# Kernel optimization log

Hardware: AMD Instinct MI355X
Metric: run time of the kernel (lower is better)

The kernel has to match this reference:

```python
import jax, jax.numpy as jnp
import numpy as np
import math

NUM_HEADS = 12
EMBED_DIM = 768

def setup_inputs() -> dict:
    key = jax.random.key(0)
    ks = jax.random.split(key, 9)
    B, T, D = 2, 2048, EMBED_DIM
    s = 1.0 / math.sqrt(D)
    inp = {
        "x": jax.random.normal(ks[0], (B, T, D), dtype=jnp.float32),
        "Wq": jax.random.normal(ks[1], (D, D), dtype=jnp.float32) * s,
        "bq": jnp.zeros((D,), dtype=jnp.float32),
        "Wk": jax.random.normal(ks[2], (D, D), dtype=jnp.float32) * s,
        "bk": jnp.zeros((D,), dtype=jnp.float32),
        "Wv": jax.random.normal(ks[3], (D, D), dtype=jnp.float32) * s,
        "bv": jnp.zeros((D,), dtype=jnp.float32),
        "Wo": jax.random.normal(ks[4], (D, D), dtype=jnp.float32) * s,
        "bo": jnp.zeros((D,), dtype=jnp.float32),
    }
    return inp

def reference(x, Wq, bq, Wk, bk, Wv, bv, Wo, bo):
    B, T, D = x.shape
    H = NUM_HEADS
    Dh = D // H
    # QKV projections, split heads: [B, H, T, Dh]
    def proj(W, b):
        y = x @ W.T + b
        return y.reshape(B, T, H, Dh).transpose(0, 2, 1, 3)
    q = proj(Wq, bq)
    k = proj(Wk, bk)
    v = proj(Wv, bv)
    scores = jnp.einsum('bhtd,bhsd->bhts', q, k) / math.sqrt(Dh)  # [B,H,T,T]
    attn = jax.nn.softmax(scores, axis=-1)
    ctx = jnp.einsum('bhts,bhsd->bhtd', attn, v)  # [B,H,T,Dh]
    ctx = ctx.transpose(0, 2, 1, 3).reshape(B, T, D)
    out = ctx @ Wo.T + bo
    return out
```

## Files before the change

kernel.cpp:

```cpp
#include <hip/hip_runtime.h>
#include <math.h>

using f32x4   = __attribute__((ext_vector_type(4))) float;
using bf16x8  = __attribute__((ext_vector_type(8))) short;

constexpr int Bb = 2;
constexpr int T  = 2048;
constexpr int D  = 768;
constexpr int H  = 12;
constexpr int Dh = 64;
constexpr int M  = Bb * T;
constexpr int NQKV = 3 * D;
#define SCALE_Q 0.18033688011112042f

__device__ __forceinline__ unsigned short f2bf(float f) {
    unsigned u = __float_as_uint(f);
    u += 0x7fffu + ((u >> 16) & 1u);
    return (unsigned short)(u >> 16);
}

__device__ __forceinline__ ushort4 f2bf4(float4 f) {
    return make_ushort4(f2bf(f.x), f2bf(f.y), f2bf(f.z), f2bf(f.w));
}

__device__ __forceinline__ unsigned permpk(float hi_f, float lo_f) {
    return __builtin_amdgcn_perm(__float_as_uint(hi_f), __float_as_uint(lo_f),
                                 0x07060302u);
}

__device__ __forceinline__ void async_copy16(const void* g, void* lds_base) {
    __builtin_amdgcn_global_load_lds(
        (const __attribute__((address_space(1))) unsigned int*)g,
        (__attribute__((address_space(3))) unsigned int*)lds_base, 16, 0, 0);
}

__global__ __launch_bounds__(256) void prep_kernel(
    const float4* __restrict__ x,
    const float4* __restrict__ Wq, const float4* __restrict__ Wk,
    const float4* __restrict__ Wv, const float4* __restrict__ Wo,
    const float* __restrict__ bq, const float* __restrict__ bk, const float* __restrict__ bv,
    ushort4* __restrict__ Xb, ushort4* __restrict__ Wqkvb, ushort4* __restrict__ Wob,
    float* __restrict__ biasS)
{
    const int stride = gridDim.x * 256;
    const int i0 = blockIdx.x * 256 + threadIdx.x;
    const int NX = M * D / 4;
    const int NW = D * D / 4;
    for (int i = i0; i < NX; i += stride) Xb[i] = f2bf4(x[i]);
    for (int i = i0; i < NW; i += stride) {
        Wqkvb[i]          = f2bf4(Wq[i]);
        Wqkvb[NW + i]     = f2bf4(Wk[i]);
        Wqkvb[2 * NW + i] = f2bf4(Wv[i]);
        Wob[i]            = f2bf4(Wo[i]);
    }
    for (int i = i0; i < D; i += stride) {
        biasS[i]         = bq[i];
        biasS[D + i]     = bk[i];
        biasS[2 * D + i] = bv[i];
    }
}

template <int MODE, int TM>
__global__ __launch_bounds__(256) void gemm_bt_kernel(
    const unsigned short* __restrict__ A, const unsigned short* __restrict__ Bm,
    const float* __restrict__ bias, const int Kdim, const int Ndim,
    float* __restrict__ Cout,
    unsigned short* __restrict__ Qo, unsigned short* __restrict__ Ko,
    unsigned short* __restrict__ Vo)
{
    constexpr int IW  = TM / 32;
    constexpr int NCH = (TM + 128) / 8;
    __shared__ unsigned short Sm[(TM + 128) * 64];
    const int tid  = threadIdx.x;
    const int lane = tid & 63, wv = tid >> 6;
    const int l15  = lane & 15, l4 = lane >> 4;
    const int wr   = wv >> 1,  wc = wv & 1;

    const int lin = blockIdx.y * gridDim.x + blockIdx.x;
    const int gx  = (lin >> 3) % gridDim.x;
    const int gy  = (lin / (8 * gridDim.x)) * 8 + (lin & 7);
    const int row0 = gy * TM, col0 = gx * 128;

    f32x4 acc[IW][4];
    #pragma unroll
    for (int i = 0; i < IW; ++i)
        #pragma unroll
        for (int j = 0; j < 4; ++j)
            acc[i][j] = (f32x4){0.f, 0.f, 0.f, 0.f};

    for (int k0 = 0; k0 < Kdim; k0 += 64) {
        __syncthreads();
        #pragma unroll
        for (int ch0 = 0; ch0 < NCH; ch0 += 4) {
            const int ch = ch0 + wv;
            const int offb = ch * 1024;
            const int off  = offb + lane * 16;
            const int r  = off >> 7;
            const int bl = (off & 127) >> 4;
            const int gc = (bl ^ (r & 7)) << 3;
            const unsigned short* src = (r < TM)
                ? A  + (size_t)(row0 + r) * Kdim + k0 + gc
                : Bm + (size_t)(col0 + (r - TM)) * Kdim + k0 + gc;
            async_copy16(src, (char*)Sm + offb);
        }
        __syncthreads();

        #pragma unroll
        for (int c = 0; c < 2; ++c) {
            bf16x8 af[IW], bfr[4];
            #pragma unroll
            for (int i = 0; i < IW; ++i) {
                const int row = wr * (TM / 2) + i * 16 + l15;
                af[i] = *(const bf16x8*)((const char*)Sm +
                        row * 128 + (((c << 2) + l4) ^ (row & 7)) * 16);
            }
            #pragma unroll
            for (int j = 0; j < 4; ++j) {
                const int row = TM + wc * 64 + j * 16 + l15;
                bfr[j] = *(const bf16x8*)((const char*)Sm +
                        row * 128 + (((c << 2) + l4) ^ (row & 7)) * 16);
            }
            #pragma unroll
            for (int i = 0; i < IW; ++i)
                #pragma unroll
                for (int j = 0; j < 4; ++j)
                    acc[i][j] = __builtin_amdgcn_mfma_f32_16x16x32_bf16(af[i], bfr[j], acc[i][j], 0, 0, 0);
        }
    }

    if (MODE == 0) {
        #pragma unroll
        for (int j = 0; j < 4; ++j) {
            const int n = col0 + wc * 64 + j * 16 + l15;
            const float bv_ = bias[n];
            #pragma unroll
            for (int i = 0; i < IW; ++i) {
                #pragma unroll
                for (int r = 0; r < 4; ++r) {
                    const int m = row0 + wr * (TM / 2) + i * 16 + l4 * 4 + r;
                    Cout[(size_t)m * Ndim + n] = acc[i][j][r] + bv_;
                }
            }
        }
    } else {
        #pragma unroll
        for (int j = 0; j < 4; ++j) {
            const int n = col0 + wc * 64 + j * 16 + l15;
            const int which = n / D;
            const int hd = n % D;
            const int h = hd >> 6, d = hd & 63;
            const float bv_ = bias[n];
            if (which == 2) {
                #pragma unroll
                for (int i = 0; i < IW; ++i) {
                    const int m0 = row0 + wr * (TM / 2) + i * 16 + l4 * 4;
                    const int b = m0 >> 11, t = m0 & (T - 1);
                    const int g = (t >> 2) & 3, h16 = (t >> 4) & 1;
                    const int tp = (t & ~31) | (g << 3) | (h16 << 2);
                    float4 v4;
                    v4.x = acc[i][j][0] + bv_; v4.y = acc[i][j][1] + bv_;
                    v4.z = acc[i][j][2] + bv_; v4.w = acc[i][j][3] + bv_;
                    *(ushort4*)&Vo[((size_t)(b * H + h) * Dh + d) * T + tp] = f2bf4(v4);
                }
            } else {
                const float scale = (which == 0) ? SCALE_Q : 1.0f;
                unsigned short* dst = (which == 0) ? Qo : Ko;
                #pragma unroll
                for (int i = 0; i < IW; ++i) {
                    #pragma unroll
                    for (int r = 0; r < 4; ++r) {
                        const int m = row0 + wr * (TM / 2) + i * 16 + l4 * 4 + r;
                        const int b = m >> 11, t = m & (T - 1);
                        dst[((size_t)(b * H + h) * T + t) * Dh + d] =
                            f2bf((acc[i][j][r] + bv_) * scale);
                    }
                }
            }
        }
    }
}

__global__ __launch_bounds__(256) void attn_kernel(
    const unsigned short* __restrict__ Q, const unsigned short* __restrict__ Kg,
    const unsigned short* __restrict__ Vt, unsigned short* __restrict__ Ctx)
{
    __shared__ unsigned short Ks[2][64 * 64];
    __shared__ unsigned short Vs[2][64 * 64];
    const int bh = blockIdx.y;
    const int q0 = blockIdx.x * 64;
    const int tid = threadIdx.x, lane = tid & 63, wv = tid >> 6;
    const int l15 = lane & 15, l4 = lane >> 4;
    const unsigned short* Qp = Q  + (size_t)bh * T * Dh;
    const unsigned short* Kp = Kg + (size_t)bh * T * Dh;
    const unsigned short* Vp = Vt + (size_t)bh * Dh * T;

    bf16x8 qf[2];
    #pragma unroll
    for (int c = 0; c < 2; ++c)
        qf[c] = *(const bf16x8*)&Qp[(size_t)(q0 + wv * 16 + l15) * Dh + c * 32 + l4 * 8];

    const short oneb = (short)0x3F80;
    const bf16x8 onesf = {oneb, oneb, oneb, oneb, oneb, oneb, oneb, oneb};

    auto load_tiles = [&](int kt, int buf) {
        #pragma unroll
        for (int i = 0; i < 2; ++i) {
            const int offb = wv * 2048 + i * 1024;
            const int off  = offb + lane * 16;
            const int r = off >> 7;
            const int blk = (off & 127) >> 4;
            const int gc = (blk ^ (r & 7)) << 3;
            async_copy16(Kp + (size_t)(kt + r) * Dh + gc, (char*)&Ks[buf][0] + offb);
            async_copy16(Vp + (size_t)r * T + kt + gc,    (char*)&Vs[buf][0] + offb);
        }
    };

    load_tiles(0, 0);
    f32x4 o[4], oL;
    #pragma unroll
    for (int nj = 0; nj < 4; ++nj) o[nj] = (f32x4){0.f, 0.f, 0.f, 0.f};
    oL = (f32x4){0.f, 0.f, 0.f, 0.f};

    for (int kt64 = 0; kt64 < T / 64; ++kt64) {
        const int cur = kt64 & 1;
        __syncthreads();
        if (kt64 + 1 < T / 64) load_tiles((kt64 + 1) * 64, cur ^ 1);

        const char* Kb = (const char*)&Ks[cur][0];
        const char* Vb = (const char*)&Vs[cur][0];

        f32x4 Sa[2] = {(f32x4){0.f,0.f,0.f,0.f}, (f32x4){0.f,0.f,0.f,0.f}};
        #pragma unroll
        for (int c = 0; c < 2; ++c) {
            #pragma unroll
            for (int t = 0; t < 2; ++t) {
                const int row = t * 16 + l15;
                bf16x8 kb = *(const bf16x8*)(Kb + row * 128 + (((c << 2) + l4) ^ (row & 7)) * 16);
                Sa[t] = __builtin_amdgcn_mfma_f32_16x16x32_bf16(kb, qf[c], Sa[t], 0, 0, 0);
            }
        }
        #pragma unroll
        for (int t = 0; t < 2; ++t)
            #pragma unroll
            for (int r = 0; r < 4; ++r)
                Sa[t][r] = __builtin_amdgcn_exp2f(Sa[t][r]);
        union { unsigned u[4]; bf16x8 v; } p0;
        p0.u[0] = permpk(Sa[0][1], Sa[0][0]);
        p0.u[1] = permpk(Sa[0][3], Sa[0][2]);
        p0.u[2] = permpk(Sa[1][1], Sa[1][0]);
        p0.u[3] = permpk(Sa[1][3], Sa[1][2]);

        f32x4 Sb[2] = {(f32x4){0.f,0.f,0.f,0.f}, (f32x4){0.f,0.f,0.f,0.f}};
        #pragma unroll
        for (int c = 0; c < 2; ++c) {
            #pragma unroll
            for (int t = 0; t < 2; ++t) {
                const int row = (t + 2) * 16 + l15;
                bf16x8 kb = *(const bf16x8*)(Kb + row * 128 + (((c << 2) + l4) ^ (row & 7)) * 16);
                Sb[t] = __builtin_amdgcn_mfma_f32_16x16x32_bf16(kb, qf[c], Sb[t], 0, 0, 0);
            }
        }

        oL = __builtin_amdgcn_mfma_f32_16x16x32_bf16(p0.v, onesf, oL, 0, 0, 0);
        #pragma unroll
        for (int nj = 0; nj < 4; ++nj) {
            const int row = nj * 16 + l15;
            bf16x8 vb = *(const bf16x8*)(Vb + row * 128 + ((l4) ^ (row & 7)) * 16);
            o[nj] = __builtin_amdgcn_mfma_f32_16x16x32_bf16(p0.v, vb, o[nj], 0, 0, 0);
        }

        #pragma unroll
        for (int t = 0; t < 2; ++t)
            #pragma unroll
            for (int r = 0; r < 4; ++r)
                Sb[t][r] = __builtin_amdgcn_exp2f(Sb[t][r]);
        union { unsigned u[4]; bf16x8 v; } p1;
        p1.u[0] = permpk(Sb[0][1], Sb[0][0]);
        p1.u[1] = permpk(Sb[0][3], Sb[0][2]);
        p1.u[2] = permpk(Sb[1][1], Sb[1][0]);
        p1.u[3] = permpk(Sb[1][3], Sb[1][2]);

        oL = __builtin_amdgcn_mfma_f32_16x16x32_bf16(p1.v, onesf, oL, 0, 0, 0);
        #pragma unroll
        for (int nj = 0; nj < 4; ++nj) {
            const int row = nj * 16 + l15;
            bf16x8 vb = *(const bf16x8*)(Vb + row * 128 + ((4 + l4) ^ (row & 7)) * 16);
            o[nj] = __builtin_amdgcn_mfma_f32_16x16x32_bf16(p1.v, vb, o[nj], 0, 0, 0);
        }
    }

    const int b = bh / H, h = bh % H;
    #pragma unroll
    for (int r = 0; r < 4; ++r) {
        const float inv = 1.0f / oL[r];
        const int t = q0 + wv * 16 + l4 * 4 + r;
        #pragma unroll
        for (int nj = 0; nj < 4; ++nj) {
            const int col = h * 64 + nj * 16 + l15;
            Ctx[(size_t)(b * T + t) * D + col] = f2bf(o[nj][r] * inv);
        }
    }
}

extern "C" void kernel_launch(void* const* d_in, const int* in_sizes, int n_in,
                              void* d_out, int out_size, void* d_ws, size_t ws_size,
                              hipStream_t stream) {
    const float* x  = (const float*)d_in[0];
    const float* Wq = (const float*)d_in[1];
    const float* bq = (const float*)d_in[2];
    const float* Wk = (const float*)d_in[3];
    const float* bk = (const float*)d_in[4];
    const float* Wv = (const float*)d_in[5];
    const float* bv = (const float*)d_in[6];
    const float* Wo = (const float*)d_in[7];
    const float* bo = (const float*)d_in[8];
    float* out = (float*)d_out;

    char* w = (char*)d_ws;
    auto alloc = [&](size_t bytes) {
        char* p = w; w += (bytes + 255) & ~(size_t)255; return p;
    };
    unsigned short* Xb    = (unsigned short*)alloc((size_t)M * D * 2);
    unsigned short* Wqkvb = (unsigned short*)alloc((size_t)NQKV * D * 2);
    unsigned short* Wob   = (unsigned short*)alloc((size_t)D * D * 2);
    float*          biasS = (float*)alloc((size_t)NQKV * 4);
    unsigned short* Qb    = (unsigned short*)alloc((size_t)M * D * 2);
    unsigned short* Kb    = (unsigned short*)alloc((size_t)M * D * 2);
    unsigned short* Vtb   = (unsigned short*)alloc((size_t)M * D * 2);
    unsigned short* Ctxb  = (unsigned short*)alloc((size_t)M * D * 2);

    prep_kernel<<<1024, 256, 0, stream>>>(
        (const float4*)x, (const float4*)Wq, (const float4*)Wk, (const float4*)Wv,
        (const float4*)Wo, bq, bk, bv,
        (ushort4*)Xb, (ushort4*)Wqkvb, (ushort4*)Wob, biasS);

    gemm_bt_kernel<1, 128><<<dim3(NQKV / 128, M / 128), 256, 0, stream>>>(
        Xb, Wqkvb, biasS, D, NQKV, nullptr, Qb, Kb, Vtb);

    attn_kernel<<<dim3(T / 64, Bb * H), 256, 0, stream>>>(Qb, Kb, Vtb, Ctxb);

    gemm_bt_kernel<0, 128><<<dim3(D / 128, M / 128), 256, 0, stream>>>(
        Ctxb, Wob, bo, D, D, out, nullptr, nullptr, nullptr);
}
```

Baseline: 162.7 us.

## Process two query groups per wave in attention to reuse K/V fragments

Each wave in the attention kernel now handles 32 query rows as two 16-row groups, so every K and V fragment read from LDS feeds two MFMAs. The block covers 128 queries, halving the grid and the K/V global loads per query. The output projection GEMM switches to a 64-row tile to add blocks. The cost is more accumulator registers per wave, which may lower occupancy, and fewer attention blocks (384) to spread across the CUs.

```diff
diff --git a/kernel.cpp b/kernel.cpp
--- a/kernel.cpp
+++ b/kernel.cpp
@@ -187,17 +187,19 @@
     __shared__ unsigned short Ks[2][64 * 64];
     __shared__ unsigned short Vs[2][64 * 64];
     const int bh = blockIdx.y;
-    const int q0 = blockIdx.x * 64;
+    const int q0 = blockIdx.x * 128;
     const int tid = threadIdx.x, lane = tid & 63, wv = tid >> 6;
     const int l15 = lane & 15, l4 = lane >> 4;
     const unsigned short* Qp = Q  + (size_t)bh * T * Dh;
     const unsigned short* Kp = Kg + (size_t)bh * T * Dh;
     const unsigned short* Vp = Vt + (size_t)bh * Dh * T;
 
-    bf16x8 qf[2];
+    bf16x8 qf[2][2];
     #pragma unroll
-    for (int c = 0; c < 2; ++c)
-        qf[c] = *(const bf16x8*)&Qp[(size_t)(q0 + wv * 16 + l15) * Dh + c * 32 + l4 * 8];
+    for (int qg = 0; qg < 2; ++qg)
+        #pragma unroll
+        for (int c = 0; c < 2; ++c)
+            qf[qg][c] = *(const bf16x8*)&Qp[(size_t)(q0 + wv * 32 + qg * 16 + l15) * Dh + c * 32 + l4 * 8];
 
     const short oneb = (short)0x3F80;
     const bf16x8 onesf = {oneb, oneb, oneb, oneb, oneb, oneb, oneb, oneb};
@@ -216,10 +218,13 @@
     };
 
     load_tiles(0, 0);
-    f32x4 o[4], oL;
+    f32x4 o[2][4], oL[2];
     #pragma unroll
-    for (int nj = 0; nj < 4; ++nj) o[nj] = (f32x4){0.f, 0.f, 0.f, 0.f};
-    oL = (f32x4){0.f, 0.f, 0.f, 0.f};
+    for (int qg = 0; qg < 2; ++qg) {
+        #pragma unroll
+        for (int nj = 0; nj < 4; ++nj) o[qg][nj] = (f32x4){0.f, 0.f, 0.f, 0.f};
+        oL[qg] = (f32x4){0.f, 0.f, 0.f, 0.f};
+    }
 
     for (int kt64 = 0; kt64 < T / 64; ++kt64) {
         const int cur = kt64 & 1;
@@ -229,75 +234,110 @@
         const char* Kb = (const char*)&Ks[cur][0];
         const char* Vb = (const char*)&Vs[cur][0];
 
-        f32x4 Sa[2] = {(f32x4){0.f,0.f,0.f,0.f}, (f32x4){0.f,0.f,0.f,0.f}};
+        f32x4 Sa[2][2];
+        #pragma unroll
+        for (int t = 0; t < 2; ++t)
+            #pragma unroll
+            for (int qg = 0; qg < 2; ++qg)
+                Sa[t][qg] = (f32x4){0.f, 0.f, 0.f, 0.f};
         #pragma unroll
         for (int c = 0; c < 2; ++c) {
             #pragma unroll
             for (int t = 0; t < 2; ++t) {
                 const int row = t * 16 + l15;
                 bf16x8 kb = *(const bf16x8*)(Kb + row * 128 + (((c << 2) + l4) ^ (row & 7)) * 16);
-                Sa[t] = __builtin_amdgcn_mfma_f32_16x16x32_bf16(kb, qf[c], Sa[t], 0, 0, 0);
+                #pragma unroll
+                for (int qg = 0; qg < 2; ++qg)
+                    Sa[t][qg] = __builtin_amdgcn_mfma_f32_16x16x32_bf16(kb, qf[qg][c], Sa[t][qg], 0, 0, 0);
             }
         }
         #pragma unroll
         for (int t = 0; t < 2; ++t)
             #pragma unroll
-            for (int r = 0; r < 4; ++r)
-                Sa[t][r] = __builtin_amdgcn_exp2f(Sa[t][r]);
-        union { unsigned u[4]; bf16x8 v; } p0;
-        p0.u[0] = permpk(Sa[0][1], Sa[0][0]);
-        p0.u[1] = permpk(Sa[0][3], Sa[0][2]);
-        p0.u[2] = permpk(Sa[1][1], Sa[1][0]);
-        p0.u[3] = permpk(Sa[1][3], Sa[1][2]);
-
-        f32x4 Sb[2] = {(f32x4){0.f,0.f,0.f,0.f}, (f32x4){0.f,0.f,0.f,0.f}};
+            for (int qg = 0; qg < 2; ++qg)
+                #pragma unroll
+                for (int r = 0; r < 4; ++r)
+                    Sa[t][qg][r] = __builtin_amdgcn_exp2f(Sa[t][qg][r]);
+        union { unsigned u[4]; bf16x8 v; } p0[2];
+        #pragma unroll
+        for (int qg = 0; qg < 2; ++qg) {
+            p0[qg].u[0] = permpk(Sa[0][qg][1], Sa[0][qg][0]);
+            p0[qg].u[1] = permpk(Sa[0][qg][3], Sa[0][qg][2]);
+            p0[qg].u[2] = permpk(Sa[1][qg][1], Sa[1][qg][0]);
+            p0[qg].u[3] = permpk(Sa[1][qg][3], Sa[1][qg][2]);
+        }
+
+        f32x4 Sb[2][2];
+        #pragma unroll
+        for (int t = 0; t < 2; ++t)
+            #pragma unroll
+            for (int qg = 0; qg < 2; ++qg)
+                Sb[t][qg] = (f32x4){0.f, 0.f, 0.f, 0.f};
         #pragma unroll
         for (int c = 0; c < 2; ++c) {
             #pragma unroll
             for (int t = 0; t < 2; ++t) {
                 const int row = (t + 2) * 16 + l15;
                 bf16x8 kb = *(const bf16x8*)(Kb + row * 128 + (((c << 2) + l4) ^ (row & 7)) * 16);
-                Sb[t] = __builtin_amdgcn_mfma_f32_16x16x32_bf16(kb, qf[c], Sb[t], 0, 0, 0);
-            }
-        }
-
-        oL = __builtin_amdgcn_mfma_f32_16x16x32_bf16(p0.v, onesf, oL, 0, 0, 0);
+                #pragma unroll
+                for (int qg = 0; qg < 2; ++qg)
+                    Sb[t][qg] = __builtin_amdgcn_mfma_f32_16x16x32_bf16(kb, qf[qg][c], Sb[t][qg], 0, 0, 0);
+            }
+        }
+
+        #pragma unroll
+        for (int qg = 0; qg < 2; ++qg)
+            oL[qg] = __builtin_amdgcn_mfma_f32_16x16x32_bf16(p0[qg].v, onesf, oL[qg], 0, 0, 0);
         #pragma unroll
         for (int nj = 0; nj < 4; ++nj) {
             const int row = nj * 16 + l15;
             bf16x8 vb = *(const bf16x8*)(Vb + row * 128 + ((l4) ^ (row & 7)) * 16);
-            o[nj] = __builtin_amdgcn_mfma_f32_16x16x32_bf16(p0.v, vb, o[nj], 0, 0, 0);
+            #pragma unroll
+            for (int qg = 0; qg < 2; ++qg)
+                o[qg][nj] = __builtin_amdgcn_mfma_f32_16x16x32_bf16(p0[qg].v, vb, o[qg][nj], 0, 0, 0);
         }
 
         #pragma unroll
         for (int t = 0; t < 2; ++t)
             #pragma unroll
-            for (int r = 0; r < 4; ++r)
-                Sb[t][r] = __builtin_amdgcn_exp2f(Sb[t][r]);
-        union { unsigned u[4]; bf16x8 v; } p1;
-        p1.u[0] = permpk(Sb[0][1], Sb[0][0]);
-        p1.u[1] = permpk(Sb[0][3], Sb[0][2]);
-        p1.u[2] = permpk(Sb[1][1], Sb[1][0]);
-        p1.u[3] = permpk(Sb[1][3], Sb[1][2]);
-
-        oL = __builtin_amdgcn_mfma_f32_16x16x32_bf16(p1.v, onesf, oL, 0, 0, 0);
+            for (int qg = 0; qg < 2; ++qg)
+                #pragma unroll
+                for (int r = 0; r < 4; ++r)
+                    Sb[t][qg][r] = __builtin_amdgcn_exp2f(Sb[t][qg][r]);
+        union { unsigned u[4]; bf16x8 v; } p1[2];
+        #pragma unroll
+        for (int qg = 0; qg < 2; ++qg) {
+            p1[qg].u[0] = permpk(Sb[0][qg][1], Sb[0][qg][0]);
+            p1[qg].u[1] = permpk(Sb[0][qg][3], Sb[0][qg][2]);
+            p1[qg].u[2] = permpk(Sb[1][qg][1], Sb[1][qg][0]);
+            p1[qg].u[3] = permpk(Sb[1][qg][3], Sb[1][qg][2]);
+        }
+
+        #pragma unroll
+        for (int qg = 0; qg < 2; ++qg)
+            oL[qg] = __builtin_amdgcn_mfma_f32_16x16x32_bf16(p1[qg].v, onesf, oL[qg], 0, 0, 0);
         #pragma unroll
         for (int nj = 0; nj < 4; ++nj) {
             const int row = nj * 16 + l15;
             bf16x8 vb = *(const bf16x8*)(Vb + row * 128 + ((4 + l4) ^ (row & 7)) * 16);
-            o[nj] = __builtin_amdgcn_mfma_f32_16x16x32_bf16(p1.v, vb, o[nj], 0, 0, 0);
+            #pragma unroll
+            for (int qg = 0; qg < 2; ++qg)
+                o[qg][nj] = __builtin_amdgcn_mfma_f32_16x16x32_bf16(p1[qg].v, vb, o[qg][nj], 0, 0, 0);
         }
     }
 
     const int b = bh / H, h = bh % H;
     #pragma unroll
-    for (int r = 0; r < 4; ++r) {
-        const float inv = 1.0f / oL[r];
-        const int t = q0 + wv * 16 + l4 * 4 + r;
-        #pragma unroll
-        for (int nj = 0; nj < 4; ++nj) {
-            const int col = h * 64 + nj * 16 + l15;
-            Ctx[(size_t)(b * T + t) * D + col] = f2bf(o[nj][r] * inv);
+    for (int qg = 0; qg < 2; ++qg) {
+        #pragma unroll
+        for (int r = 0; r < 4; ++r) {
+            const float inv = 1.0f / oL[qg][r];
+            const int t = q0 + wv * 32 + qg * 16 + l4 * 4 + r;
+            #pragma unroll
+            for (int nj = 0; nj < 4; ++nj) {
+                const int col = h * 64 + nj * 16 + l15;
+                Ctx[(size_t)(b * T + t) * D + col] = f2bf(o[qg][nj][r] * inv);
+            }
         }
     }
 }
@@ -337,8 +377,8 @@
     gemm_bt_kernel<1, 128><<<dim3(NQKV / 128, M / 128), 256, 0, stream>>>(
         Xb, Wqkvb, biasS, D, NQKV, nullptr, Qb, Kb, Vtb);
 
-    attn_kernel<<<dim3(T / 64, Bb * H), 256, 0, stream>>>(Qb, Kb, Vtb, Ctxb);
-
-    gemm_bt_kernel<0, 128><<<dim3(D / 128, M / 128), 256, 0, stream>>>(
+    attn_kernel<<<dim3(T / 128, Bb * H), 256, 0, stream>>>(Qb, Kb, Vtb, Ctxb);
+
+    gemm_bt_kernel<0, 64><<<dim3(D / 128, M / 64), 256, 0, stream>>>(
         Ctxb, Wob, bo, D, D, out, nullptr, nullptr, nullptr);
 }
```

Result: slower. 168.5 us (+3.6%).
